# Kernel tuning notes

Measured on AMD Instinct MI355X. Metric: run time of the kernel, lower is better.

The kernel has to match this reference:

```python
import jax, jax.numpy as jnp
import numpy as np

D_MODEL = 2048
HQ = 32          # query heads
HKV = 8          # kv heads
HD = D_MODEL // HQ   # head_dim = 64
G = HQ // HKV        # group size = 4
THETA = 10000.0


def _rope(x, pos):
    """x: (B, H, T, D), pos: (B, T) int. Rotates even/odd interleaved pairs."""
    D = x.shape[-1]
    inv_freq = THETA ** (-jnp.arange(0, D, 2, dtype=jnp.float32) / D)   # (D/2,)
    ang = pos[:, None, :, None].astype(jnp.float32) * inv_freq          # (B,1,T,D/2)
    cos, sin = jnp.cos(ang), jnp.sin(ang)
    x1, x2 = x[..., 0::2], x[..., 1::2]
    r1 = x1 * cos - x2 * sin
    r2 = x1 * sin + x2 * cos
    return jnp.stack([r1, r2], axis=-1).reshape(x.shape)


def setup_inputs() -> dict:
    key = jax.random.key(0)
    ks = jax.random.split(key, 5)
    B, T = 2, 2048
    s = lambda fan_in: 1.0 / np.sqrt(fan_in)
    return {
        "x": jax.random.normal(ks[0], (B, T, D_MODEL), jnp.float32),
        "token_positions": jnp.arange(T, dtype=jnp.int32),
        "WQ": jax.random.normal(ks[1], (HQ * HD, D_MODEL), jnp.float32) * s(D_MODEL),
        "WK": jax.random.normal(ks[2], (HKV * HD, D_MODEL), jnp.float32) * s(D_MODEL),
        "WV": jax.random.normal(ks[3], (HKV * HD, D_MODEL), jnp.float32) * s(D_MODEL),
        "WO": jax.random.normal(ks[4], (D_MODEL, HQ * HD), jnp.float32) * s(HQ * HD),
    }


def reference(x, token_positions, WQ, WK, WV, WO):
    B, T, _ = x.shape
    pos = token_positions if token_positions.ndim == 2 else jnp.broadcast_to(token_positions[None, :], (B, T))

    # Projections (Linear is y = x @ W.T, no bias)
    Q = (x @ WQ.T).reshape(B, T, HQ, HD).transpose(0, 2, 1, 3)    # (B,Hq,T,D)
    K = (x @ WK.T).reshape(B, T, HKV, HD).transpose(0, 2, 1, 3)   # (B,Hkv,T,D)
    V = (x @ WV.T).reshape(B, T, HKV, HD).transpose(0, 2, 1, 3)

    Q = _rope(Q, pos)
    K = _rope(K, pos)

    # GQA: group query heads per kv head instead of duplicating K/V
    Qg = Q.reshape(B, HKV, G, T, HD)
    scale = jnp.float32(1.0 / np.sqrt(HD))
    scores = jnp.einsum('bkgqd,bkld->bkgql', Qg, K) * scale       # (B,Hkv,G,T,T)

    causal = jnp.tril(jnp.ones((T, T), dtype=bool))
    scores = jnp.where(causal, scores, jnp.finfo(scores.dtype).min)
    A = jax.nn.softmax(scores, axis=-1)

    O = jnp.einsum('bkgql,bkld->bkgqd', A, V)                     # (B,Hkv,G,T,D)
    O = O.reshape(B, HQ, T, HD).transpose(0, 2, 1, 3).reshape(B, T, HQ * HD)
    return O @ WO.T
```

## Files before the change

kernel.cpp:

```cpp
#include <hip/hip_runtime.h>
#include <hip/hip_bf16.h>

#define B_   2
#define T_   2048
#define DM_  2048
#define HQ_  32
#define HKV_ 8
#define HD_  64

typedef __attribute__((ext_vector_type(8))) short bf16x8;
typedef __attribute__((ext_vector_type(4))) float f32x4;
typedef __fp16 f16x4 __attribute__((ext_vector_type(4)));
typedef __fp16 f16x2 __attribute__((ext_vector_type(2)));

__device__ __forceinline__ unsigned short f2bf(float f) {
    unsigned int u = __float_as_uint(f);
    u = (u + 0x7fffu + ((u >> 16) & 1u)) >> 16;
    return (unsigned short)u;
}

__device__ __forceinline__ void gload16(const unsigned short* g, unsigned short* l) {
    __builtin_amdgcn_global_load_lds(
        (const __attribute__((address_space(1))) unsigned int*)g,
        (__attribute__((address_space(3))) unsigned int*)l, 16, 0, 0);
}


#define CONV_N 4718592

__global__ __launch_bounds__(256) void convert_all(
    const float* __restrict__ x,  const float* __restrict__ WQ,
    const float* __restrict__ WK, const float* __restrict__ WV,
    const float* __restrict__ WO, unsigned short* __restrict__ ws,
    const int* __restrict__ pos,  float* __restrict__ trig)
{
    int i = blockIdx.x*256 + threadIdx.x;
    if (i >= CONV_N) {
        int j = i - CONV_N;
        if (j < T_*32) {
            int t = j >> 5, p = j & 31;
            float inv = exp2f(-0.4152410118609203f * (float)p);
            float ang = (float)pos[t] * inv;
            float sn, cs;
            sincosf(ang, &sn, &cs);
            *(float2*)&trig[j*2] = make_float2(cs, sn);
        }
        return;
    }
    const float* src; unsigned short* dst; int rel;
    if (i < 2097152)      { src = x;  dst = ws;                 rel = i; }
    else if (i < 3145728) { src = WQ; dst = ws + 8388608;       rel = i - 2097152; }
    else if (i < 3407872) { src = WK; dst = ws + 8388608+4194304; rel = i - 3145728; }
    else if (i < 3670016) { src = WV; dst = ws + 8388608+5242880; rel = i - 3407872; }
    else                  { src = WO; dst = ws + 14680064;      rel = i - 3670016; }
    float4 v = *(const float4*)(src + (size_t)rel*4);
    uint2 pk;
    pk.x = (unsigned int)f2bf(v.x) | ((unsigned int)f2bf(v.y) << 16);
    pk.y = (unsigned int)f2bf(v.z) | ((unsigned int)f2bf(v.w) << 16);
    *(uint2*)(dst + (size_t)rel*4) = pk;
}

__global__ __launch_bounds__(256) void qkv_gemm_bf16(
    const unsigned short* __restrict__ Ab, const unsigned short* __restrict__ Wb,
    unsigned short* __restrict__ Qb, unsigned short* __restrict__ Kb,
    unsigned short* __restrict__ Vt, const float* __restrict__ trig)
{
    __shared__ unsigned short As[3][128*32];
    __shared__ unsigned short Bs[3][128*32];
    const int tid  = threadIdx.x;
    const int ln   = tid & 63;
    const int wv   = tid >> 6;
    const int wm   = (wv >> 1) * 64;
    const int wn   = (wv & 1) * 64;
    const int col  = ln & 15;
    const int quad = ln >> 4;

    const int bid = blockIdx.x;
    const int swz = (bid & 7) * 96 + (bid >> 3);
    const int n0  = (swz % 24) * 128;
    const int m0  = (swz / 24) * 128;

    const int cg = ((tid & 3) ^ ((tid >> 3) & 3)) * 8;
    const unsigned short* aG = Ab + (size_t)(m0 + (tid>>2))*DM_ + cg;
    const unsigned short* bG = Wb + (size_t)(n0 + (tid>>2))*DM_ + cg;
    const int ck = (quad ^ ((col >> 1) & 3)) * 8;

    f32x4 acc[4][4];
    #pragma unroll
    for (int i=0;i<4;++i)
        #pragma unroll
        for (int j=0;j<4;++j) { acc[i][j][0]=0.f; acc[i][j][1]=0.f; acc[i][j][2]=0.f; acc[i][j][3]=0.f; }

    auto stage = [&](int buf, int k0) {
        unsigned short* aL = &As[buf][wv*512];
        unsigned short* bL = &Bs[buf][wv*512];
        gload16(aG + k0,                  aL);
        gload16(aG + (size_t)64*DM_ + k0, aL + 2048);
        gload16(bG + k0,                  bL);
        gload16(bG + (size_t)64*DM_ + k0, bL + 2048);
    };

    auto kstep = [&](int bc, int k0v, int bstage, bool dostage, bool last) {
        if (last) asm volatile("s_waitcnt vmcnt(0)" ::: "memory");
        else      asm volatile("s_waitcnt vmcnt(4)" ::: "memory");
        __builtin_amdgcn_s_barrier();
        if (dostage) stage(bstage, k0v + 64);
        const unsigned short* Ac = As[bc];
        const unsigned short* Bc = Bs[bc];
        bf16x8 af[4], bfr[4];
        #pragma unroll
        for (int i2=0;i2<4;++i2) {
            af[i2]  = *(const bf16x8*)&Ac[(wm + i2*16 + col)*32 + ck];
            bfr[i2] = *(const bf16x8*)&Bc[(wn + i2*16 + col)*32 + ck];
        }
        #pragma unroll
        for (int i2=0;i2<4;++i2)
            #pragma unroll
            for (int j2=0;j2<4;++j2)
                acc[i2][j2] = __builtin_amdgcn_mfma_f32_16x16x32_bf16(af[i2], bfr[j2], acc[i2][j2], 0, 0, 0);
    };

    stage(0, 0);
    stage(1, 32);

    int k0 = 0;
    for (int rep = 0; rep < 20; ++rep) {
        kstep(0, k0,      2, true, false);
        kstep(1, k0+32,   0, true, false);
        kstep(2, k0+64,   1, true, false);
        k0 += 96;
    }
    kstep(0, 1920, 2, true,  false);
    kstep(1, 1952, 0, true,  false);
    kstep(2, 1984, 1, false, false);
    kstep(0, 2016, 0, false, true);

    const int b  = m0 >> 11;
    const int tb = m0 & 2047;
    #pragma unroll
    for (int j=0;j<4;++j) {
        const int n = n0 + wn + j*16 + col;
        if (n < 2560) {
            const int d   = n & 63;
            const int p   = d >> 1;
            const bool ev = (d & 1) == 0;
            const float sc = (n < 2048) ? 0.18033688011112042f : 1.0f;
            unsigned short* outp = (n < 2048)
                ? Qb + (((size_t)(b*HQ_  + (n>>6)))*T_)*HD_
                : Kb + (((size_t)(b*HKV_ + ((n-2048)>>6)))*T_)*HD_;
            #pragma unroll
            for (int i=0;i<4;++i) {
                const int t0 = tb + wm + i*16 + quad*4;
                #pragma unroll
                for (int r=0;r<4;++r) {
                    float self = acc[i][j][r];
                    float part = __shfl_xor(self, 1);
                    float2 cs  = *(const float2*)&trig[((t0 + r)*32 + p)*2];
                    float out  = ev ? (self*cs.x - part*cs.y)
                                    : (part*cs.y + self*cs.x);
                    out *= sc;
                    unsigned int pk = (unsigned int)f2bf(out);
                    unsigned int po = __shfl_xor(pk, 1);
                    if (ev)
                        *(unsigned int*)(outp + (size_t)(t0 + r)*HD_ + d) = pk | (po << 16);
                }
            }
        } else {
            #pragma unroll
            for (int i=0;i<4;++i) {
                const int t = tb + wm + i*16 + quad*4;
                unsigned short* vp = Vt + (((size_t)(b*HKV_ + ((n-2560)>>6)))*HD_ + (n&63))*T_ + t;
                union { f16x2 h; unsigned int u; } c0, c1;
                c0.h = __builtin_amdgcn_cvt_pkrtz(acc[i][j][0], acc[i][j][1]);
                c1.h = __builtin_amdgcn_cvt_pkrtz(acc[i][j][2], acc[i][j][3]);
                *(unsigned int*)(vp)     = c0.u;
                *(unsigned int*)(vp + 2) = c1.u;
            }
        }
    }
}

__global__ __launch_bounds__(512, 4) void attn_mfma(
    const unsigned short* __restrict__ Qb, const unsigned short* __restrict__ Kb,
    const unsigned short* __restrict__ Vh, unsigned short* __restrict__ Ob)
{
    __shared__ unsigned short Ks[2][64*64];
    __shared__ unsigned short Vs[2][64*64];

    const int tid  = threadIdx.x;
    const int lane = tid & 63;
    const int wv   = tid >> 6;
    const int q16  = lane & 15;
    const int quad = lane >> 4;
    const int bxi  = blockIdx.x;
    const int bh   = blockIdx.y;
    const int b    = bh >> 5;
    const int h    = bh & 31;
    const int kvh  = h >> 2;
    const int qa   = bxi;
    const int qbt  = 31 - bxi;
    const bool isB = (wv < 4);
    const int  kact = isB ? qbt : qa;
    const int  myq  = (isB ? qbt*64 + wv*16 : qa*64 + (wv-4)*16) + q16;

    const unsigned short* kbase = Kb + ((size_t)(b*HKV_ + kvh))*T_*HD_;
    const unsigned short* vbase = Vh + ((size_t)(b*HKV_ + kvh))*(size_t)HD_*T_;

    const bf16x8 q0 = *(const bf16x8*)(Qb + ((size_t)bh*T_ + myq)*HD_ + quad*8);
    const bf16x8 q1 = *(const bf16x8*)(Qb + ((size_t)bh*T_ + myq)*HD_ + 32 + quad*8);

    f32x4 o[4];
    #pragma unroll
    for (int i=0;i<4;++i) { o[i][0]=0.f; o[i][1]=0.f; o[i][2]=0.f; o[i][3]=0.f; }
    float l = 0.f;

    const int sr = tid >> 3;
    const int sj = tid & 7;
    const int sc = (sj ^ (sr & 7)) * 8;

    const int rk7 = q16 & 7;
    const int ck0 = (quad ^ rk7) * 8;
    const int ck1 = ((quad + 4) ^ rk7) * 8;

    auto smrow = [&](const f32x4 s, float& ps) -> f16x4 {
        float e0 = exp2f(s[0]), e1 = exp2f(s[1]);
        float e2 = exp2f(s[2]), e3 = exp2f(s[3]);
        ps += (e0+e1) + (e2+e3);
        union { f16x2 hh[2]; f16x4 v; } c;
        c.hh[0] = __builtin_amdgcn_cvt_pkrtz(e0, e1);
        c.hh[1] = __builtin_amdgcn_cvt_pkrtz(e2, e3);
        return c.v;
    };

    auto tile_barrier = [&]() {
        asm volatile("s_waitcnt lgkmcnt(0)" ::: "memory");
        __builtin_amdgcn_s_barrier();
        __builtin_amdgcn_sched_barrier(0);
    };

    uint4 kr, vr;
    kr = *(const uint4*)(kbase + (size_t)sr*HD_ + sj*8);
    vr = *(const uint4*)(vbase + (size_t)sr*T_ + sj*8);
    *(uint4*)&Ks[0][sr*64 + sc] = kr;
    *(uint4*)&Vs[0][sr*64 + sc] = vr;
    kr = *(const uint4*)(kbase + (size_t)(64+sr)*HD_ + sj*8);
    vr = *(const uint4*)(vbase + (size_t)sr*T_ + 64 + sj*8);
    __syncthreads();

    int cur = 0;
    for (int kt = 0; kt <= qbt; ++kt) {
        const int nxt = cur ^ 1;
        if (kt <= kact) {
            const unsigned short* KsC = Ks[cur];
            const unsigned short* VsC = Vs[cur];
            f32x4 s[4];
            #pragma unroll
            for (int t=0;t<4;++t) { s[t][0]=0.f; s[t][1]=0.f; s[t][2]=0.f; s[t][3]=0.f; }

            __builtin_amdgcn_s_setprio(1);
            #pragma unroll
            for (int t = 0; t < 4; ++t) {
                const int rk = (t*16 + q16) * 64;
                bf16x8 a0 = *(const bf16x8*)&KsC[rk + ck0];
                bf16x8 a1 = *(const bf16x8*)&KsC[rk + ck1];
                s[t] = __builtin_amdgcn_mfma_f32_16x16x32_bf16(a0, q0, s[t], 0, 0, 0);
                s[t] = __builtin_amdgcn_mfma_f32_16x16x32_bf16(a1, q1, s[t], 0, 0, 0);
            }
            if (kt == kact) {
                #pragma unroll
                for (int t = 0; t < 4; ++t)
                    #pragma unroll
                    for (int r = 0; r < 4; ++r)
                        if (kt*64 + t*16 + quad*4 + r > myq) s[t][r] = -1e30f;
            }
            f16x4 pf[4];
            float ps = 0.f;
            #pragma unroll
            for (int t = 0; t < 4; ++t) pf[t] = smrow(s[t], ps);
            #pragma unroll
            for (int t = 0; t < 4; ++t) {
                const int cv = ((2*t + (quad>>1)) ^ rk7) * 8 + (quad&1)*4;
                #pragma unroll
                for (int dt=0;dt<4;++dt) {
                    f16x4 va = *(const f16x4*)&VsC[(dt*16 + q16)*64 + cv];
                    o[dt] = __builtin_amdgcn_mfma_f32_16x16x16f16(va, pf[t], o[dt], 0, 0, 0);
                }
            }
            __builtin_amdgcn_s_setprio(0);
            l += ps;
        }
        if (kt < qbt) {
            *(uint4*)&Ks[nxt][sr*64 + sc] = kr;
            *(uint4*)&Vs[nxt][sr*64 + sc] = vr;
        }
        if (kt + 1 < qbt) {
            const int kn = (kt+2)*64;
            kr = *(const uint4*)(kbase + (size_t)(kn+sr)*HD_ + sj*8);
            vr = *(const uint4*)(vbase + (size_t)sr*T_ + kn + sj*8);
        }
        tile_barrier();
        cur ^= 1;
    }

    l += __shfl_xor(l, 16); l += __shfl_xor(l, 32);
    const float rl = 1.0f / l;
    unsigned short* op = Ob + ((size_t)(b*T_ + myq))*(HQ_*HD_) + h*HD_;
    #pragma unroll
    for (int dt = 0; dt < 4; ++dt) {
        uint2 pk;
        pk.x = (unsigned int)f2bf(o[dt][0]*rl) | ((unsigned int)f2bf(o[dt][1]*rl) << 16);
        pk.y = (unsigned int)f2bf(o[dt][2]*rl) | ((unsigned int)f2bf(o[dt][3]*rl) << 16);
        *(uint2*)(op + dt*16 + quad*4) = pk;
    }
}

__global__ __launch_bounds__(256) void out_gemm_bf16(
    const unsigned short* __restrict__ Ab, const unsigned short* __restrict__ Wb,
    float* __restrict__ C)
{
    __shared__ unsigned short As[3][128*32];
    __shared__ unsigned short Bs[3][128*32];
    const int tid  = threadIdx.x;
    const int ln   = tid & 63;
    const int wv   = tid >> 6;
    const int wm   = (wv >> 1) * 64;
    const int wn   = (wv & 1) * 64;
    const int col  = ln & 15;
    const int quad = ln >> 4;

    const int bid = blockIdx.x;
    const int swz = (bid & 7) * 64 + (bid >> 3);
    const int n0  = (swz & 15) * 128;
    const int m0  = (swz >> 4) * 128;

    const int cg = ((tid & 3) ^ ((tid >> 3) & 3)) * 8;
    const unsigned short* aG = Ab + (size_t)(m0 + (tid>>2))*DM_ + cg;
    const unsigned short* bG = Wb + (size_t)(n0 + (tid>>2))*DM_ + cg;
    const int ck = (quad ^ ((col >> 1) & 3)) * 8;

    f32x4 acc[4][4];
    #pragma unroll
    for (int i=0;i<4;++i)
        #pragma unroll
        for (int j=0;j<4;++j) { acc[i][j][0]=0.f; acc[i][j][1]=0.f; acc[i][j][2]=0.f; acc[i][j][3]=0.f; }

    auto stage = [&](int buf, int k0) {
        unsigned short* aL = &As[buf][wv*512];
        unsigned short* bL = &Bs[buf][wv*512];
        gload16(aG + k0,                  aL);
        gload16(aG + (size_t)64*DM_ + k0, aL + 2048);
        gload16(bG + k0,                  bL);
        gload16(bG + (size_t)64*DM_ + k0, bL + 2048);
    };

    auto kstep = [&](int bc, int k0v, int bstage, bool dostage, bool last) {
        if (last) asm volatile("s_waitcnt vmcnt(0)" ::: "memory");
        else      asm volatile("s_waitcnt vmcnt(4)" ::: "memory");
        __builtin_amdgcn_s_barrier();
        if (dostage) stage(bstage, k0v + 64);
        const unsigned short* Ac = As[bc];
        const unsigned short* Bc = Bs[bc];
        bf16x8 af[4], bfr[4];
        #pragma unroll
        for (int i2=0;i2<4;++i2) {
            af[i2]  = *(const bf16x8*)&Ac[(wm + i2*16 + col)*32 + ck];
            bfr[i2] = *(const bf16x8*)&Bc[(wn + i2*16 + col)*32 + ck];
        }
        #pragma unroll
        for (int i2=0;i2<4;++i2)
            #pragma unroll
            for (int j2=0;j2<4;++j2)
                acc[i2][j2] = __builtin_amdgcn_mfma_f32_16x16x32_bf16(af[i2], bfr[j2], acc[i2][j2], 0, 0, 0);
    };

    stage(0, 0);
    stage(1, 32);

    int k0 = 0;
    for (int rep = 0; rep < 20; ++rep) {
        kstep(0, k0,      2, true, false);
        kstep(1, k0+32,   0, true, false);
        kstep(2, k0+64,   1, true, false);
        k0 += 96;
    }
    kstep(0, 1920, 2, true,  false);
    kstep(1, 1952, 0, true,  false);
    kstep(2, 1984, 1, false, false);
    kstep(0, 2016, 0, false, true);

    #pragma unroll
    for (int i=0;i<4;++i) {
        const int m = m0 + wm + i*16 + quad*4;
        #pragma unroll
        for (int j=0;j<4;++j) {
            const int n = n0 + wn + j*16 + col;
            #pragma unroll
            for (int r=0;r<4;++r)
                C[(size_t)(m + r)*DM_ + n] = acc[i][j][r];
        }
    }
}

extern "C" void kernel_launch(void* const* d_in, const int* in_sizes, int n_in,
                              void* d_out, int out_size, void* d_ws, size_t ws_size,
                              hipStream_t stream) {
    const float* x   = (const float*)d_in[0];
    const int*   pos = (const int*)  d_in[1];
    const float* WQ  = (const float*)d_in[2];
    const float* WK  = (const float*)d_in[3];
    const float* WV  = (const float*)d_in[4];
    const float* WO  = (const float*)d_in[5];
    float* out = (float*)d_out;

    unsigned short* xb  = (unsigned short*)d_ws;
    unsigned short* Wb  = xb  + (size_t)8388608;
    unsigned short* WOb = Wb  + (size_t)6291456;
    unsigned short* Qb  = WOb + (size_t)4194304;
    unsigned short* Kb  = Qb  + (size_t)8388608;
    unsigned short* Vt  = Kb  + (size_t)2097152;
    unsigned short* Ob  = Vt  + (size_t)2097152;
    float* trig = (float*)Ob;

    convert_all<<<18688, 256, 0, stream>>>(x, WQ, WK, WV, WO, (unsigned short*)d_ws, pos, trig);

    qkv_gemm_bf16<<<768, 256, 0, stream>>>(xb, Wb, Qb, Kb, Vt, trig);

    dim3 g3(16, B_*HQ_);
    attn_mfma<<<g3, 512, 0, stream>>>(Qb, Kb, Vt, Ob);

    out_gemm_bf16<<<512, 256, 0, stream>>>(Ob, WOb, out);
}
```

Measured before the change: 311.8 us.

## Process four strided query tiles per block to reuse each K/V tile

The attention kernel now gives each 256-thread block four query tiles (g, g+8, g+16, g+24) instead of two paired tiles in a 512-thread block. Each K/V tile loaded into shared memory is reused across up to four query tiles, and tiles drop out as the causal boundary passes them. This cuts K/V global and shared-memory traffic per query and balances causal work across blocks. In exchange it uses four times the accumulator registers per wave, halves the grid to 512 blocks, and uses launch bounds of 2 blocks, which lowers occupancy and parallelism.

Result: faster. 304.7 us (-2.3%).

```diff
diff --git a/kernel.cpp b/kernel.cpp
--- a/kernel.cpp
+++ b/kernel.cpp
@@ -180,7 +180,17 @@
     }
 }
 
-__global__ __launch_bounds__(512, 4) void attn_mfma(
+__device__ __forceinline__ f16x4 smrow_fn(const f32x4 s, float& ps) {
+    float e0 = exp2f(s[0]), e1 = exp2f(s[1]);
+    float e2 = exp2f(s[2]), e3 = exp2f(s[3]);
+    ps += (e0+e1) + (e2+e3);
+    union { f16x2 hh[2]; f16x4 v; } c;
+    c.hh[0] = __builtin_amdgcn_cvt_pkrtz(e0, e1);
+    c.hh[1] = __builtin_amdgcn_cvt_pkrtz(e2, e3);
+    return c.v;
+}
+
+__global__ __launch_bounds__(256, 2) void attn_mfma(
     const unsigned short* __restrict__ Qb, const unsigned short* __restrict__ Kb,
     const unsigned short* __restrict__ Vh, unsigned short* __restrict__ Ob)
 {
@@ -189,30 +199,36 @@
 
     const int tid  = threadIdx.x;
     const int lane = tid & 63;
-    const int wv   = tid >> 6;
+    const int wave = tid >> 6;
     const int q16  = lane & 15;
     const int quad = lane >> 4;
-    const int bxi  = blockIdx.x;
+    const int g    = 7 - blockIdx.x;
     const int bh   = blockIdx.y;
     const int b    = bh >> 5;
     const int h    = bh & 31;
     const int kvh  = h >> 2;
-    const int qa   = bxi;
-    const int qbt  = 31 - bxi;
-    const bool isB = (wv < 4);
-    const int  kact = isB ? qbt : qa;
-    const int  myq  = (isB ? qbt*64 + wv*16 : qa*64 + (wv-4)*16) + q16;
+    const int q3t  = g + 24;
 
     const unsigned short* kbase = Kb + ((size_t)(b*HKV_ + kvh))*T_*HD_;
     const unsigned short* vbase = Vh + ((size_t)(b*HKV_ + kvh))*(size_t)HD_*T_;
 
-    const bf16x8 q0 = *(const bf16x8*)(Qb + ((size_t)bh*T_ + myq)*HD_ + quad*8);
-    const bf16x8 q1 = *(const bf16x8*)(Qb + ((size_t)bh*T_ + myq)*HD_ + 32 + quad*8);
-
-    f32x4 o[4];
-    #pragma unroll
-    for (int i=0;i<4;++i) { o[i][0]=0.f; o[i][1]=0.f; o[i][2]=0.f; o[i][3]=0.f; }
-    float l = 0.f;
+    int qg[4];
+    bf16x8 qf0[4], qf1[4];
+    #pragma unroll
+    for (int s=0;s<4;++s) {
+        qg[s]  = (g + 8*s)*64 + wave*16 + q16;
+        qf0[s] = *(const bf16x8*)(Qb + ((size_t)bh*T_ + qg[s])*HD_ + quad*8);
+        qf1[s] = *(const bf16x8*)(Qb + ((size_t)bh*T_ + qg[s])*HD_ + 32 + quad*8);
+    }
+
+    f32x4 o[4][4];
+    float l[4];
+    #pragma unroll
+    for (int s=0;s<4;++s) {
+        l[s] = 0.f;
+        #pragma unroll
+        for (int dt=0;dt<4;++dt) { o[s][dt][0]=0.f; o[s][dt][1]=0.f; o[s][dt][2]=0.f; o[s][dt][3]=0.f; }
+    }
 
     const int sr = tid >> 3;
     const int sj = tid & 7;
@@ -221,16 +237,6 @@
     const int rk7 = q16 & 7;
     const int ck0 = (quad ^ rk7) * 8;
     const int ck1 = ((quad + 4) ^ rk7) * 8;
-
-    auto smrow = [&](const f32x4 s, float& ps) -> f16x4 {
-        float e0 = exp2f(s[0]), e1 = exp2f(s[1]);
-        float e2 = exp2f(s[2]), e3 = exp2f(s[3]);
-        ps += (e0+e1) + (e2+e3);
-        union { f16x2 hh[2]; f16x4 v; } c;
-        c.hh[0] = __builtin_amdgcn_cvt_pkrtz(e0, e1);
-        c.hh[1] = __builtin_amdgcn_cvt_pkrtz(e2, e3);
-        return c.v;
-    };
 
     auto tile_barrier = [&]() {
         asm volatile("s_waitcnt lgkmcnt(0)" ::: "memory");
@@ -238,79 +244,114 @@
         __builtin_amdgcn_sched_barrier(0);
     };
 
-    uint4 kr, vr;
-    kr = *(const uint4*)(kbase + (size_t)sr*HD_ + sj*8);
-    vr = *(const uint4*)(vbase + (size_t)sr*T_ + sj*8);
-    *(uint4*)&Ks[0][sr*64 + sc] = kr;
-    *(uint4*)&Vs[0][sr*64 + sc] = vr;
-    kr = *(const uint4*)(kbase + (size_t)(64+sr)*HD_ + sj*8);
-    vr = *(const uint4*)(vbase + (size_t)sr*T_ + 64 + sj*8);
+    uint4 kr0, kr1, vr0, vr1;
+    kr0 = *(const uint4*)(kbase + (size_t)sr*HD_ + sj*8);
+    kr1 = *(const uint4*)(kbase + (size_t)(sr+32)*HD_ + sj*8);
+    vr0 = *(const uint4*)(vbase + (size_t)sr*T_ + sj*8);
+    vr1 = *(const uint4*)(vbase + (size_t)(sr+32)*T_ + sj*8);
+    *(uint4*)&Ks[0][sr*64 + sc]      = kr0;
+    *(uint4*)&Ks[0][(sr+32)*64 + sc] = kr1;
+    *(uint4*)&Vs[0][sr*64 + sc]      = vr0;
+    *(uint4*)&Vs[0][(sr+32)*64 + sc] = vr1;
+    kr0 = *(const uint4*)(kbase + (size_t)(64+sr)*HD_ + sj*8);
+    kr1 = *(const uint4*)(kbase + (size_t)(64+sr+32)*HD_ + sj*8);
+    vr0 = *(const uint4*)(vbase + (size_t)sr*T_ + 64 + sj*8);
+    vr1 = *(const uint4*)(vbase + (size_t)(sr+32)*T_ + 64 + sj*8);
     __syncthreads();
 
     int cur = 0;
-    for (int kt = 0; kt <= qbt; ++kt) {
-        const int nxt = cur ^ 1;
-        if (kt <= kact) {
-            const unsigned short* KsC = Ks[cur];
-            const unsigned short* VsC = Vs[cur];
-            f32x4 s[4];
-            #pragma unroll
-            for (int t=0;t<4;++t) { s[t][0]=0.f; s[t][1]=0.f; s[t][2]=0.f; s[t][3]=0.f; }
-
-            __builtin_amdgcn_s_setprio(1);
-            #pragma unroll
-            for (int t = 0; t < 4; ++t) {
-                const int rk = (t*16 + q16) * 64;
-                bf16x8 a0 = *(const bf16x8*)&KsC[rk + ck0];
-                bf16x8 a1 = *(const bf16x8*)&KsC[rk + ck1];
-                s[t] = __builtin_amdgcn_mfma_f32_16x16x32_bf16(a0, q0, s[t], 0, 0, 0);
-                s[t] = __builtin_amdgcn_mfma_f32_16x16x32_bf16(a1, q1, s[t], 0, 0, 0);
-            }
-            if (kt == kact) {
-                #pragma unroll
-                for (int t = 0; t < 4; ++t)
-                    #pragma unroll
-                    for (int r = 0; r < 4; ++r)
-                        if (kt*64 + t*16 + quad*4 + r > myq) s[t][r] = -1e30f;
-            }
-            f16x4 pf[4];
-            float ps = 0.f;
-            #pragma unroll
-            for (int t = 0; t < 4; ++t) pf[t] = smrow(s[t], ps);
-            #pragma unroll
-            for (int t = 0; t < 4; ++t) {
-                const int cv = ((2*t + (quad>>1)) ^ rk7) * 8 + (quad&1)*4;
-                #pragma unroll
-                for (int dt=0;dt<4;++dt) {
-                    f16x4 va = *(const f16x4*)&VsC[(dt*16 + q16)*64 + cv];
-                    o[dt] = __builtin_amdgcn_mfma_f32_16x16x16f16(va, pf[t], o[dt], 0, 0, 0);
-                }
-            }
-            __builtin_amdgcn_s_setprio(0);
-            l += ps;
-        }
-        if (kt < qbt) {
-            *(uint4*)&Ks[nxt][sr*64 + sc] = kr;
-            *(uint4*)&Vs[nxt][sr*64 + sc] = vr;
-        }
-        if (kt + 1 < qbt) {
-            const int kn = (kt+2)*64;
-            kr = *(const uint4*)(kbase + (size_t)(kn+sr)*HD_ + sj*8);
-            vr = *(const uint4*)(vbase + (size_t)sr*T_ + kn + sj*8);
-        }
-        tile_barrier();
-        cur ^= 1;
-    }
-
-    l += __shfl_xor(l, 16); l += __shfl_xor(l, 32);
-    const float rl = 1.0f / l;
-    unsigned short* op = Ob + ((size_t)(b*T_ + myq))*(HQ_*HD_) + h*HD_;
-    #pragma unroll
-    for (int dt = 0; dt < 4; ++dt) {
-        uint2 pk;
-        pk.x = (unsigned int)f2bf(o[dt][0]*rl) | ((unsigned int)f2bf(o[dt][1]*rl) << 16);
-        pk.y = (unsigned int)f2bf(o[dt][2]*rl) | ((unsigned int)f2bf(o[dt][3]*rl) << 16);
-        *(uint2*)(op + dt*16 + quad*4) = pk;
+    int kt  = 0;
+
+#define TILE_BODY(NS, QEND)                                                    \
+  {                                                                            \
+    const unsigned short* KsC = Ks[cur];                                       \
+    const unsigned short* VsC = Vs[cur];                                       \
+    const int nxt = cur ^ 1;                                                   \
+    f32x4 sS[4][4];                                                            \
+    _Pragma("unroll")                                                          \
+    for (int s=4-(NS);s<4;++s)                                                 \
+      _Pragma("unroll")                                                        \
+      for (int t=0;t<4;++t) { sS[s][t][0]=0.f; sS[s][t][1]=0.f;                \
+                              sS[s][t][2]=0.f; sS[s][t][3]=0.f; }              \
+    __builtin_amdgcn_s_setprio(1);                                             \
+    _Pragma("unroll")                                                          \
+    for (int t=0;t<4;++t) {                                                    \
+      const int rk = (t*16 + q16) * 64;                                        \
+      bf16x8 a0 = *(const bf16x8*)&KsC[rk + ck0];                              \
+      bf16x8 a1 = *(const bf16x8*)&KsC[rk + ck1];                              \
+      _Pragma("unroll")                                                        \
+      for (int s=4-(NS);s<4;++s) {                                             \
+        sS[s][t] = __builtin_amdgcn_mfma_f32_16x16x32_bf16(a0, qf0[s], sS[s][t], 0, 0, 0); \
+        sS[s][t] = __builtin_amdgcn_mfma_f32_16x16x32_bf16(a1, qf1[s], sS[s][t], 0, 0, 0); \
+      }                                                                        \
+    }                                                                          \
+    if (kt < q3t) {                                                            \
+      *(uint4*)&Ks[nxt][sr*64 + sc]      = kr0;                                \
+      *(uint4*)&Ks[nxt][(sr+32)*64 + sc] = kr1;                                \
+      *(uint4*)&Vs[nxt][sr*64 + sc]      = vr0;                                \
+      *(uint4*)&Vs[nxt][(sr+32)*64 + sc] = vr1;                                \
+    }                                                                          \
+    if (kt + 1 < q3t) {                                                        \
+      const int kn = (kt+2)*64;                                                \
+      kr0 = *(const uint4*)(kbase + (size_t)(kn+sr)*HD_ + sj*8);               \
+      kr1 = *(const uint4*)(kbase + (size_t)(kn+sr+32)*HD_ + sj*8);            \
+      vr0 = *(const uint4*)(vbase + (size_t)sr*T_ + kn + sj*8);                \
+      vr1 = *(const uint4*)(vbase + (size_t)(sr+32)*T_ + kn + sj*8);           \
+    }                                                                          \
+    if (kt == (QEND)) {                               \
+      const int s0 = 4-(NS);                                                   \
+      _Pragma("unroll")                                                        \
+      for (int t=0;t<4;++t)                                                    \
+        _Pragma("unroll")                                                      \
+        for (int r=0;r<4;++r)                                                  \
+          if (kt*64 + t*16 + quad*4 + r > qg[s0]) sS[s0][t][r] = -1e30f;       \
+    }                                                                          \
+    f16x4 pf[4][4];                                                            \
+    _Pragma("unroll")                                                          \
+    for (int s=4-(NS);s<4;++s) {                                               \
+      float ps = 0.f;                                                          \
+      _Pragma("unroll")                                                        \
+      for (int t=0;t<4;++t) pf[s][t] = smrow_fn(sS[s][t], ps);                 \
+      l[s] += ps;                                                              \
+    }                                                                          \
+    _Pragma("unroll")                                                          \
+    for (int t=0;t<4;++t) {                                                    \
+      const int cv = ((2*t + (quad>>1)) ^ rk7) * 8 + (quad&1)*4;               \
+      f16x4 va[4];                                                             \
+      _Pragma("unroll")                                                        \
+      for (int dt=0;dt<4;++dt)                                                 \
+        va[dt] = *(const f16x4*)&VsC[(dt*16 + q16)*64 + cv];                   \
+      _Pragma("unroll")                                                        \
+      for (int s=4-(NS);s<4;++s)                                               \
+        _Pragma("unroll")                                                      \
+        for (int dt=0;dt<4;++dt)                                               \
+          o[s][dt] = __builtin_amdgcn_mfma_f32_16x16x16f16(va[dt], pf[s][t], o[s][dt], 0, 0, 0); \
+    }                                                                          \
+    __builtin_amdgcn_s_setprio(0);                                             \
+    tile_barrier();                                                            \
+    cur ^= 1;                                                                  \
+  }
+
+    for (; kt <= g;      ++kt) TILE_BODY(4, g)
+    for (; kt <= g + 8;  ++kt) TILE_BODY(3, g + 8)
+    for (; kt <= g + 16; ++kt) TILE_BODY(2, g + 16)
+    for (; kt <= g + 24; ++kt) TILE_BODY(1, g + 24)
+
+#undef TILE_BODY
+
+    #pragma unroll
+    for (int s=0;s<4;++s) {
+        float ls = l[s];
+        ls += __shfl_xor(ls, 16); ls += __shfl_xor(ls, 32);
+        const float rl = 1.0f / ls;
+        unsigned short* op = Ob + ((size_t)(b*T_ + qg[s]))*(HQ_*HD_) + h*HD_;
+        #pragma unroll
+        for (int dt = 0; dt < 4; ++dt) {
+            uint2 pk;
+            pk.x = (unsigned int)f2bf(o[s][dt][0]*rl) | ((unsigned int)f2bf(o[s][dt][1]*rl) << 16);
+            pk.y = (unsigned int)f2bf(o[s][dt][2]*rl) | ((unsigned int)f2bf(o[s][dt][3]*rl) << 16);
+            *(uint2*)(op + dt*16 + quad*4) = pk;
+        }
     }
 }
 
@@ -425,8 +466,8 @@
 
     qkv_gemm_bf16<<<768, 256, 0, stream>>>(xb, Wb, Qb, Kb, Vt, trig);
 
-    dim3 g3(16, B_*HQ_);
-    attn_mfma<<<g3, 512, 0, stream>>>(Qb, Kb, Vt, Ob);
+    dim3 g3(8, B_*HQ_);
+    attn_mfma<<<g3, 256, 0, stream>>>(Qb, Kb, Vt, Ob);
 
     out_gemm_bf16<<<512, 256, 0, stream>>>(Ob, WOb, out);
 }
```
